# Kernel optimization log

Hardware: AMD Instinct MI355X
Metric: run time of the kernel (lower is better)

The kernel has to match this reference:

```python
import jax, jax.numpy as jnp
import numpy as np

EPS = 1e-6

def _ln(x):
    # LayerNorm without affine, eps=1e-6
    mu = jnp.mean(x, axis=-1, keepdims=True)
    var = jnp.var(x, axis=-1, keepdims=True)
    return (x - mu) * jax.lax.rsqrt(var + EPS)

def setup_inputs() -> dict:
    key = jax.random.key(0)
    ks = jax.random.split(key, 12)
    B, N, C = 8, 1024, 768
    H = 12
    Hf = 4 * C  # mlp hidden
    s = 0.02
    return {
        "x": jax.random.normal(ks[0], (B, N, C), jnp.float32),
        "c": jax.random.normal(ks[1], (B, C), jnp.float32),
        "qkv_w": jax.random.normal(ks[2], (3 * C, C), jnp.float32) * s,
        "qkv_b": jax.random.normal(ks[3], (3 * C,), jnp.float32) * s,
        "proj_w": jax.random.normal(ks[4], (C, C), jnp.float32) * s,
        "proj_b": jax.random.normal(ks[5], (C,), jnp.float32) * s,
        "fc1_w": jax.random.normal(ks[6], (Hf, C), jnp.float32) * s,
        "fc1_b": jax.random.normal(ks[7], (Hf,), jnp.float32) * s,
        "fc2_w": jax.random.normal(ks[8], (C, Hf), jnp.float32) * s,
        "fc2_b": jax.random.normal(ks[9], (C,), jnp.float32) * s,
        "ada_w": jax.random.normal(ks[10], (6 * C, C), jnp.float32) * s,
        "ada_b": jax.random.normal(ks[11], (6 * C,), jnp.float32) * s,
    }

def reference(x, c, qkv_w, qkv_b, proj_w, proj_b, fc1_w, fc1_b, fc2_w, fc2_b, ada_w, ada_b):
    B, N, C = x.shape
    H = 12
    D = C // H
    scale = D ** -0.5

    # adaLN_modulation: SiLU then Linear -> chunk into 6 [B, C] pieces
    ada = jax.nn.silu(c) @ ada_w.T + ada_b  # [B, 6C]
    sh_msa, sc_msa, g_msa, sh_mlp, sc_mlp, g_mlp = jnp.split(ada, 6, axis=1)

    def modulate(h, shift, scale_):
        return h * (1 + scale_[:, None, :]) + shift[:, None, :]

    # --- attention branch ---
    h = modulate(_ln(x), sh_msa, sc_msa)
    qkv = h @ qkv_w.T + qkv_b                       # [B, N, 3C]
    qkv = qkv.reshape(B, N, 3, H, D)
    q, k, v = qkv[:, :, 0], qkv[:, :, 1], qkv[:, :, 2]   # [B, N, H, D]
    attn = jnp.einsum('bnhd,bmhd->bhnm', q, k) * scale   # [B, H, N, N]
    attn = jax.nn.softmax(attn, axis=-1)
    o = jnp.einsum('bhnm,bmhd->bnhd', attn, v).reshape(B, N, C)
    o = o @ proj_w.T + proj_b
    x = x + g_msa[:, None, :] * o

    # --- MLP branch ---
    h = modulate(_ln(x), sh_mlp, sc_mlp)
    h = jax.nn.gelu(h @ fc1_w.T + fc1_b, approximate=False)
    h = h @ fc2_w.T + fc2_b
    x = x + g_mlp[:, None, :] * h
    return x
```

## Files before the change

kernel.cpp:

```cpp
#include <hip/hip_runtime.h>
#include <hip/hip_bf16.h>
#include <math.h>

typedef __attribute__((ext_vector_type(8))) short bf16x8;
typedef __attribute__((ext_vector_type(4))) float f32x4;

__device__ __forceinline__ unsigned short f2bf(float f) {
  union { float f; unsigned int u; } v; v.f = f;
  unsigned int u = v.u;
  u += 0x7fffu + ((u >> 16) & 1u);
  return (unsigned short)(u >> 16);
}

__device__ __forceinline__ void gl2l16(const unsigned short* g, unsigned short* l) {
  __builtin_amdgcn_global_load_lds(
      (const __attribute__((address_space(1))) unsigned int*)g,
      (__attribute__((address_space(3))) unsigned int*)l, 16, 0, 0);
}

__device__ __forceinline__ float gelu_fast(float v) {
  float arg = v * (1.59576912f + 0.07135481f * v * v);
  return v / (1.f + __expf(-arg));
}

__global__ __launch_bounds__(256) void k_conv(const float4* __restrict__ s0, ushort4* __restrict__ d0,
                                              const float4* __restrict__ s1, ushort4* __restrict__ d1,
                                              const float4* __restrict__ s2, ushort4* __restrict__ d2,
                                              const float4* __restrict__ s3, ushort4* __restrict__ d3) {
  int i = blockIdx.x * 256 + threadIdx.x;
  const float4* s; ushort4* d; int off;
  if (i < 442368) { s = s0; d = d0; off = i; }
  else if (i < 589824) { s = s1; d = d1; off = i - 442368; }
  else if (i < 1179648) { s = s2; d = d2; off = i - 589824; }
  else { s = s3; d = d3; off = i - 1179648; }
  float4 f = s[off];
  ushort4 o;
  o.x = f2bf(f.x); o.y = f2bf(f.y); o.z = f2bf(f.z); o.w = f2bf(f.w);
  d[off] = o;
}

__global__ __launch_bounds__(256) void k_ada(const float* __restrict__ c,
                                             const float* __restrict__ ada_w,
                                             const float* __restrict__ ada_b,
                                             float* __restrict__ ada) {
  __shared__ float sc[8 * 768];
  __shared__ float red[4][64][8];
  const int t = threadIdx.x;
  for (int i = t; i < 8 * 768; i += 256) {
    float v = c[i];
    sc[i] = v / (1.f + __expf(-v));
  }
  __syncthreads();
  const int cl = t & 63, ks = t >> 6;
  const int col = blockIdx.x * 64 + cl;
  float acc[8];
#pragma unroll
  for (int b = 0; b < 8; b++) acc[b] = 0.f;
  const float* wr = ada_w + (size_t)col * 768 + ks * 192;
  for (int k = 0; k < 192; k += 4) {
    float4 w = *(const float4*)&wr[k];
    const int kk = ks * 192 + k;
#pragma unroll
    for (int b = 0; b < 8; b++) {
      acc[b] += sc[b * 768 + kk] * w.x + sc[b * 768 + kk + 1] * w.y +
                sc[b * 768 + kk + 2] * w.z + sc[b * 768 + kk + 3] * w.w;
    }
  }
#pragma unroll
  for (int b = 0; b < 8; b++) red[ks][cl][b] = acc[b];
  __syncthreads();
  if (ks == 0) {
    const float bj = ada_b[col];
#pragma unroll
    for (int b = 0; b < 8; b++)
      ada[b * 4608 + col] = red[0][cl][b] + red[1][cl][b] + red[2][cl][b] + red[3][cl][b] + bj;
  }
}

__global__ __launch_bounds__(256) void k_ln_mod(const float* __restrict__ x,
                                                const float* __restrict__ ada,
                                                int sh_off, int sc_off,
                                                unsigned short* __restrict__ h) {
  const int row = blockIdx.x, t = threadIdx.x, b = row >> 10;
  const float* xr = x + (size_t)row * 768;
  float v0 = xr[t], v1 = xr[t + 256], v2 = xr[t + 512];
  float s = v0 + v1 + v2;
  float ss = v0 * v0 + v1 * v1 + v2 * v2;
#pragma unroll
  for (int m = 1; m < 64; m <<= 1) {
    s += __shfl_xor(s, m);
    ss += __shfl_xor(ss, m);
  }
  __shared__ float red[8];
  if ((t & 63) == 0) { red[t >> 6] = s; red[4 + (t >> 6)] = ss; }
  __syncthreads();
  const float S = red[0] + red[1] + red[2] + red[3];
  const float SS = red[4] + red[5] + red[6] + red[7];
  const float mean = S * (1.f / 768.f);
  const float var = SS * (1.f / 768.f) - mean * mean;
  const float inv = rsqrtf(var + 1e-6f);
  const float* sh = ada + b * 4608 + sh_off;
  const float* scp = ada + b * 4608 + sc_off;
  unsigned short* hr = h + (size_t)row * 768;
  float vv[3] = {v0, v1, v2};
#pragma unroll
  for (int i = 0; i < 3; i++) {
    int cx = t + i * 256;
    float hh = (vv[i] - mean) * inv;
    hh = hh * (1.f + scp[cx]) + sh[cx];
    hr[cx] = f2bf(hh);
  }
}

template <int EPI, int TN>
__global__ __launch_bounds__(256) void k_gemm(const unsigned short* __restrict__ A,
                                              const unsigned short* __restrict__ B,
                                              const float* __restrict__ bias,
                                              int N, int K, int nbx,
                                              const float* __restrict__ resid,
                                              const float* __restrict__ ada, int goff,
                                              float* __restrict__ outf,
                                              unsigned short* __restrict__ outb,
                                              unsigned short* __restrict__ vt) {
  constexpr int MI = (TN == 128) ? 4 : 2;
  __shared__ __align__(16) unsigned short Asm[2][128 * 32];
  __shared__ __align__(16) unsigned short Bsm[2][TN * 32];
  const int t = threadIdx.x;
  const int w = t >> 6, lane = t & 63, l = lane & 15, qd = lane >> 4;

  const int id = blockIdx.x;
  const int xcd = id & 7, jj = id >> 3;
  const int jm = jj / nbx;
  const int bmi = xcd + (jm << 3);
  const int bni = jj - jm * nbx;
  const int bn = bni * TN, bm = bmi * 128;

  const int wm = (TN == 128) ? (w >> 1) * 64 : w * 32;
  const int wn = (TN == 128) ? (w & 1) * 64 : 0;

  const int srow = t >> 2;
  const int scol = ((t & 3) ^ ((srow >> 1) & 3)) * 8;
  const unsigned short* Ap0 = A + (size_t)(bm + srow) * K + scol;
  const unsigned short* Ap1 = A + (size_t)(bm + 64 + srow) * K + scol;
  const unsigned short* Bp0 = B + (size_t)(bn + srow) * K + scol;
  const unsigned short* Bp1 = B + (size_t)(bn + 64 + srow) * K + scol;

  f32x4 acc[MI][4];
#pragma unroll
  for (int i = 0; i < MI; i++)
#pragma unroll
    for (int j = 0; j < 4; j++) acc[i][j] = {0.f, 0.f, 0.f, 0.f};

  const int swz = (l >> 1) & 3;

  for (int k0 = 0; k0 < K; k0 += 64) {
#pragma unroll
    for (int s = 0; s < 2; s++) {
      gl2l16(Ap0 + k0 + 32 * s, &Asm[s][w * 512]);
      gl2l16(Ap1 + k0 + 32 * s, &Asm[s][2048 + w * 512]);
      gl2l16(Bp0 + k0 + 32 * s, &Bsm[s][w * 512]);
      if (TN == 128) gl2l16(Bp1 + k0 + 32 * s, &Bsm[s][2048 + w * 512]);
    }
    __syncthreads();
#pragma unroll
    for (int s = 0; s < 2; s++) {
      bf16x8 af[MI], bfr[4];
#pragma unroll
      for (int i = 0; i < MI; i++)
        af[i] = *(const bf16x8*)&Asm[s][(wm + i * 16 + l) * 32 + ((qd ^ swz) << 3)];
#pragma unroll
      for (int j = 0; j < 4; j++)
        bfr[j] = *(const bf16x8*)&Bsm[s][(wn + j * 16 + l) * 32 + ((qd ^ swz) << 3)];
#pragma unroll
      for (int i = 0; i < MI; i++)
#pragma unroll
        for (int j = 0; j < 4; j++)
          acc[i][j] = __builtin_amdgcn_mfma_f32_16x16x32_bf16(af[i], bfr[j], acc[i][j], 0, 0, 0);
    }
    __syncthreads();
  }

#pragma unroll
  for (int i = 0; i < MI; i++) {
#pragma unroll
    for (int j = 0; j < 4; j++) {
      const int gn = bn + wn + j * 16 + l;
      const float bv = bias[gn];
#pragma unroll
      for (int r = 0; r < 4; r++) {
        const int gm = bm + wm + i * 16 + qd * 4 + r;
        float v = acc[i][j][r] + bv;
        if (EPI == 0) {
          if (gn < 1536) {
            outb[(size_t)gm * 1536 + gn] = f2bf(v);
          } else {
            const int hh = (gn - 1536) >> 6, dd = (gn - 1536) & 63;
            const int bb = gm >> 10, nn = gm & 1023;
            vt[(((size_t)bb * 12 + hh) * 64 + dd) * 1024 + nn] = f2bf(v);
          }
        } else if (EPI == 2) {
          outb[(size_t)gm * N + gn] = f2bf(gelu_fast(v));
        } else {
          const int bb = gm >> 10;
          const float g = ada[bb * 4608 + goff + gn];
          outf[(size_t)gm * 768 + gn] = resid[(size_t)gm * 768 + gn] + g * v;
        }
      }
    }
  }
}

__global__ __launch_bounds__(256) void k_attn(const unsigned short* __restrict__ qk,
                                              const unsigned short* __restrict__ vt,
                                              unsigned short* __restrict__ o) {
  __shared__ __align__(16) unsigned short Ksm[64 * 76];
  __shared__ __align__(16) unsigned short Vsm[64 * 76];
  __shared__ __align__(16) unsigned short Psm[128 * 76];
  const int t = threadIdx.x;
  const int id = blockIdx.x;
  const int xcd = id & 7, j = id >> 3;
  const int bh = xcd * 12 + (j >> 3);
  const int qb = j & 7;
  const int b = bh / 12, h = bh - b * 12;
  const int w = t >> 6, lane = t & 63, l = lane & 15, qd = lane >> 4;

  const size_t qrow0 = (size_t)(b * 1024 + qb * 128 + w * 32 + l);
  bf16x8 qf[2][2];
#pragma unroll
  for (int mt = 0; mt < 2; mt++)
#pragma unroll
    for (int ks = 0; ks < 2; ks++)
      qf[mt][ks] = *(const bf16x8*)&qk[(qrow0 + mt * 16) * 1536 + h * 64 + ks * 32 + qd * 8];

  f32x4 oacc[2][4];
  float rsum[2][4];
#pragma unroll
  for (int mt = 0; mt < 2; mt++)
#pragma unroll
    for (int j2 = 0; j2 < 4; j2++) { oacc[mt][j2] = {0.f, 0.f, 0.f, 0.f}; rsum[mt][j2] = 0.f; }

  const size_t kbase = (size_t)b * 1024 * 1536 + 768 + h * 64;
  const size_t vbase = ((size_t)(b * 12 + h)) * 64 * 1024;

  for (int k0 = 0; k0 < 1024; k0 += 64) {
    for (int idx = t; idx < 512; idx += 256) {
      const int row = idx >> 3, ch = (idx & 7) * 8;
      *(bf16x8*)&Ksm[row * 76 + ch] =
          *(const bf16x8*)&qk[kbase + (size_t)(k0 + row) * 1536 + ch];
      *(bf16x8*)&Vsm[row * 76 + ch] =
          *(const bf16x8*)&vt[vbase + (size_t)row * 1024 + k0 + ch];
    }
    __syncthreads();

    bf16x8 kf[4][2];
#pragma unroll
    for (int ct = 0; ct < 4; ct++)
#pragma unroll
      for (int ks = 0; ks < 2; ks++)
        kf[ct][ks] = *(const bf16x8*)&Ksm[(ct * 16 + l) * 76 + ks * 32 + qd * 8];

#pragma unroll
    for (int mt = 0; mt < 2; mt++) {
      f32x4 s[4];
#pragma unroll
      for (int ct = 0; ct < 4; ct++) {
        f32x4 a = {0.f, 0.f, 0.f, 0.f};
        a = __builtin_amdgcn_mfma_f32_16x16x32_bf16(qf[mt][0], kf[ct][0], a, 0, 0, 0);
        a = __builtin_amdgcn_mfma_f32_16x16x32_bf16(qf[mt][1], kf[ct][1], a, 0, 0, 0);
        s[ct] = a;
      }
#pragma unroll
      for (int ct = 0; ct < 4; ct++) {
#pragma unroll
        for (int r = 0; r < 4; r++) {
          float p = __expf(s[ct][r] * 0.125f);
          rsum[mt][r] += p;
          Psm[(w * 32 + mt * 16 + qd * 4 + r) * 76 + ct * 16 + l] = f2bf(p);
        }
      }
    }

    bf16x8 vf[4][2];
#pragma unroll
    for (int dt = 0; dt < 4; dt++)
#pragma unroll
      for (int ks = 0; ks < 2; ks++)
        vf[dt][ks] = *(const bf16x8*)&Vsm[(dt * 16 + l) * 76 + ks * 32 + qd * 8];
#pragma unroll
    for (int mt = 0; mt < 2; mt++) {
      bf16x8 pf0 = *(const bf16x8*)&Psm[(w * 32 + mt * 16 + l) * 76 + qd * 8];
      bf16x8 pf1 = *(const bf16x8*)&Psm[(w * 32 + mt * 16 + l) * 76 + 32 + qd * 8];
#pragma unroll
      for (int dt = 0; dt < 4; dt++) {
        oacc[mt][dt] = __builtin_amdgcn_mfma_f32_16x16x32_bf16(pf0, vf[dt][0], oacc[mt][dt], 0, 0, 0);
        oacc[mt][dt] = __builtin_amdgcn_mfma_f32_16x16x32_bf16(pf1, vf[dt][1], oacc[mt][dt], 0, 0, 0);
      }
    }
    __syncthreads();
  }

#pragma unroll
  for (int mt = 0; mt < 2; mt++)
#pragma unroll
    for (int r = 0; r < 4; r++) {
      float rs = rsum[mt][r];
#pragma unroll
      for (int mk = 1; mk < 16; mk <<= 1) rs += __shfl_xor(rs, mk);
      const float inv = 1.f / rs;
      const size_t orow = (size_t)(b * 1024 + qb * 128 + w * 32 + mt * 16 + qd * 4 + r);
#pragma unroll
      for (int dt = 0; dt < 4; dt++)
        o[orow * 768 + h * 64 + dt * 16 + l] = f2bf(oacc[mt][dt][r] * inv);
    }
}

extern "C" void kernel_launch(void* const* d_in, const int* in_sizes, int n_in,
                              void* d_out, int out_size, void* d_ws, size_t ws_size,
                              hipStream_t stream) {
  const float* x      = (const float*)d_in[0];
  const float* c      = (const float*)d_in[1];
  const float* qkv_w  = (const float*)d_in[2];
  const float* qkv_b  = (const float*)d_in[3];
  const float* proj_w = (const float*)d_in[4];
  const float* proj_b = (const float*)d_in[5];
  const float* fc1_w  = (const float*)d_in[6];
  const float* fc1_b  = (const float*)d_in[7];
  const float* fc2_w  = (const float*)d_in[8];
  const float* fc2_b  = (const float*)d_in[9];
  const float* ada_w  = (const float*)d_in[10];
  const float* ada_b  = (const float*)d_in[11];
  float* out = (float*)d_out;

  char* ws = (char*)d_ws;
  float*          ada       = (float*)(ws + 0);
  unsigned short* qkv_w_bf  = (unsigned short*)(ws + 147456);
  unsigned short* proj_w_bf = (unsigned short*)(ws + 3686400);
  unsigned short* fc1_w_bf  = (unsigned short*)(ws + 4866048);
  unsigned short* fc2_w_bf  = (unsigned short*)(ws + 9584640);
  unsigned short* h_bf      = (unsigned short*)(ws + 14303232);
  unsigned short* qk_bf     = (unsigned short*)(ws + 26886144);
  unsigned short* vt_bf     = (unsigned short*)(ws + 52051968);
  unsigned short* o_bf      = (unsigned short*)(ws + 64634880);
  float*          x1        = (float*)(ws + 77217792);
  unsigned short* f1_bf     = qk_bf;

  k_conv<<<6912, 256, 0, stream>>>((const float4*)qkv_w, (ushort4*)qkv_w_bf,
                                   (const float4*)proj_w, (ushort4*)proj_w_bf,
                                   (const float4*)fc1_w, (ushort4*)fc1_w_bf,
                                   (const float4*)fc2_w, (ushort4*)fc2_w_bf);

  k_ada<<<72, 256, 0, stream>>>(c, ada_w, ada_b, ada);

  k_ln_mod<<<8192, 256, 0, stream>>>(x, ada, 0, 768, h_bf);

  k_gemm<0, 128><<<18 * 64, 256, 0, stream>>>(h_bf, qkv_w_bf, qkv_b, 2304, 768, 18,
                                              nullptr, nullptr, 0, nullptr, qk_bf, vt_bf);

  k_attn<<<768, 256, 0, stream>>>(qk_bf, vt_bf, o_bf);

  k_gemm<1, 64><<<12 * 64, 256, 0, stream>>>(o_bf, proj_w_bf, proj_b, 768, 768, 12,
                                             x, ada, 1536, x1, nullptr, nullptr);

  k_ln_mod<<<8192, 256, 0, stream>>>(x1, ada, 2304, 3072, h_bf);

  k_gemm<2, 128><<<24 * 64, 256, 0, stream>>>(h_bf, fc1_w_bf, fc1_b, 3072, 768, 24,
                                              nullptr, nullptr, 0, nullptr, f1_bf, nullptr);

  k_gemm<3, 64><<<12 * 64, 256, 0, stream>>>(f1_bf, fc2_w_bf, fc2_b, 768, 3072, 12,
                                             x1, ada, 3840, out, nullptr, nullptr);
}
```

Measured before the change: 421.3 us.

## Store intermediate residual in bf16, merge prologue kernels, use 3D attention grid

The intermediate residual x1 is now written and read as bf16 rather than fp32, which halves its memory traffic in the proj epilogue, the second LayerNorm and the fc2 epilogue. The weight conversion kernel and the adaLN modulation kernel are merged into one prologue launch to save a kernel launch. The attention kernel switches from XCD-aware block swizzling to a plain 3D grid. Keeping the residual in bf16 lowers the precision of the output's residual path, and dropping the swizzle may reduce L2 locality on K/V.

```diff
diff --git a/kernel.cpp b/kernel.cpp
--- a/kernel.cpp
+++ b/kernel.cpp
@@ -12,6 +12,11 @@
   return (unsigned short)(u >> 16);
 }
 
+__device__ __forceinline__ float bf2f(unsigned short h) {
+  union { unsigned int u; float f; } v; v.u = ((unsigned int)h) << 16;
+  return v.f;
+}
+
 __device__ __forceinline__ void gl2l16(const unsigned short* g, unsigned short* l) {
   __builtin_amdgcn_global_load_lds(
       (const __attribute__((address_space(1))) unsigned int*)g,
@@ -23,36 +28,38 @@
   return v / (1.f + __expf(-arg));
 }
 
-__global__ __launch_bounds__(256) void k_conv(const float4* __restrict__ s0, ushort4* __restrict__ d0,
-                                              const float4* __restrict__ s1, ushort4* __restrict__ d1,
-                                              const float4* __restrict__ s2, ushort4* __restrict__ d2,
-                                              const float4* __restrict__ s3, ushort4* __restrict__ d3) {
-  int i = blockIdx.x * 256 + threadIdx.x;
-  const float4* s; ushort4* d; int off;
-  if (i < 442368) { s = s0; d = d0; off = i; }
-  else if (i < 589824) { s = s1; d = d1; off = i - 442368; }
-  else if (i < 1179648) { s = s2; d = d2; off = i - 589824; }
-  else { s = s3; d = d3; off = i - 1179648; }
-  float4 f = s[off];
-  ushort4 o;
-  o.x = f2bf(f.x); o.y = f2bf(f.y); o.z = f2bf(f.z); o.w = f2bf(f.w);
-  d[off] = o;
-}
-
-__global__ __launch_bounds__(256) void k_ada(const float* __restrict__ c,
-                                             const float* __restrict__ ada_w,
-                                             const float* __restrict__ ada_b,
-                                             float* __restrict__ ada) {
-  __shared__ float sc[8 * 768];
-  __shared__ float red[4][64][8];
+__global__ __launch_bounds__(256) void k_prologue(
+    const float4* __restrict__ s0, ushort4* __restrict__ d0,
+    const float4* __restrict__ s1, ushort4* __restrict__ d1,
+    const float4* __restrict__ s2, ushort4* __restrict__ d2,
+    const float4* __restrict__ s3, ushort4* __restrict__ d3,
+    const float* __restrict__ c, const float* __restrict__ ada_w,
+    const float* __restrict__ ada_b, float* __restrict__ ada) {
+  __shared__ float smem[8 * 768 + 4 * 64 * 8];
   const int t = threadIdx.x;
+  const int id = blockIdx.x;
+  if (id < 6912) {
+    int i = id * 256 + t;
+    const float4* s; ushort4* d; int off;
+    if (i < 442368) { s = s0; d = d0; off = i; }
+    else if (i < 589824) { s = s1; d = d1; off = i - 442368; }
+    else if (i < 1179648) { s = s2; d = d2; off = i - 589824; }
+    else { s = s3; d = d3; off = i - 1179648; }
+    float4 f = s[off];
+    ushort4 o;
+    o.x = f2bf(f.x); o.y = f2bf(f.y); o.z = f2bf(f.z); o.w = f2bf(f.w);
+    d[off] = o;
+    return;
+  }
+  float* sc = smem;
+  float* red = smem + 8 * 768;
   for (int i = t; i < 8 * 768; i += 256) {
     float v = c[i];
     sc[i] = v / (1.f + __expf(-v));
   }
   __syncthreads();
   const int cl = t & 63, ks = t >> 6;
-  const int col = blockIdx.x * 64 + cl;
+  const int col = (id - 6912) * 64 + cl;
   float acc[8];
 #pragma unroll
   for (int b = 0; b < 8; b++) acc[b] = 0.f;
@@ -67,23 +74,31 @@
     }
   }
 #pragma unroll
-  for (int b = 0; b < 8; b++) red[ks][cl][b] = acc[b];
+  for (int b = 0; b < 8; b++) red[(ks * 64 + cl) * 8 + b] = acc[b];
   __syncthreads();
   if (ks == 0) {
     const float bj = ada_b[col];
 #pragma unroll
     for (int b = 0; b < 8; b++)
-      ada[b * 4608 + col] = red[0][cl][b] + red[1][cl][b] + red[2][cl][b] + red[3][cl][b] + bj;
-  }
-}
-
-__global__ __launch_bounds__(256) void k_ln_mod(const float* __restrict__ x,
+      ada[b * 4608 + col] = red[(0 * 64 + cl) * 8 + b] + red[(1 * 64 + cl) * 8 + b] +
+                            red[(2 * 64 + cl) * 8 + b] + red[(3 * 64 + cl) * 8 + b] + bj;
+  }
+}
+
+template <bool BF>
+__global__ __launch_bounds__(256) void k_ln_mod(const void* __restrict__ xin,
                                                 const float* __restrict__ ada,
                                                 int sh_off, int sc_off,
                                                 unsigned short* __restrict__ h) {
   const int row = blockIdx.x, t = threadIdx.x, b = row >> 10;
-  const float* xr = x + (size_t)row * 768;
-  float v0 = xr[t], v1 = xr[t + 256], v2 = xr[t + 512];
+  float v0, v1, v2;
+  if (BF) {
+    const unsigned short* xr = (const unsigned short*)xin + (size_t)row * 768;
+    v0 = bf2f(xr[t]); v1 = bf2f(xr[t + 256]); v2 = bf2f(xr[t + 512]);
+  } else {
+    const float* xr = (const float*)xin + (size_t)row * 768;
+    v0 = xr[t]; v1 = xr[t + 256]; v2 = xr[t + 512];
+  }
   float s = v0 + v1 + v2;
   float ss = v0 * v0 + v1 * v1 + v2 * v2;
 #pragma unroll
@@ -117,7 +132,8 @@
                                               const unsigned short* __restrict__ B,
                                               const float* __restrict__ bias,
                                               int N, int K, int nbx,
-                                              const float* __restrict__ resid,
+                                              const float* __restrict__ residf,
+                                              const unsigned short* __restrict__ residb,
                                               const float* __restrict__ ada, int goff,
                                               float* __restrict__ outf,
                                               unsigned short* __restrict__ outb,
@@ -198,12 +214,18 @@
             const int bb = gm >> 10, nn = gm & 1023;
             vt[(((size_t)bb * 12 + hh) * 64 + dd) * 1024 + nn] = f2bf(v);
           }
+        } else if (EPI == 1) {
+          const int bb = gm >> 10;
+          const float g = ada[bb * 4608 + goff + gn];
+          outb[(size_t)gm * 768 + gn] =
+              f2bf(residf[(size_t)gm * 768 + gn] + g * v);
         } else if (EPI == 2) {
           outb[(size_t)gm * N + gn] = f2bf(gelu_fast(v));
         } else {
           const int bb = gm >> 10;
           const float g = ada[bb * 4608 + goff + gn];
-          outf[(size_t)gm * 768 + gn] = resid[(size_t)gm * 768 + gn] + g * v;
+          outf[(size_t)gm * 768 + gn] =
+              bf2f(residb[(size_t)gm * 768 + gn]) + g * v;
         }
       }
     }
@@ -217,11 +239,7 @@
   __shared__ __align__(16) unsigned short Vsm[64 * 76];
   __shared__ __align__(16) unsigned short Psm[128 * 76];
   const int t = threadIdx.x;
-  const int id = blockIdx.x;
-  const int xcd = id & 7, j = id >> 3;
-  const int bh = xcd * 12 + (j >> 3);
-  const int qb = j & 7;
-  const int b = bh / 12, h = bh - b * 12;
+  const int qb = blockIdx.x, h = blockIdx.y, b = blockIdx.z;
   const int w = t >> 6, lane = t & 63, l = lane & 15, qd = lane >> 4;
 
   const size_t qrow0 = (size_t)(b * 1024 + qb * 128 + w * 32 + l);
@@ -341,31 +359,34 @@
   unsigned short* qk_bf     = (unsigned short*)(ws + 26886144);
   unsigned short* vt_bf     = (unsigned short*)(ws + 52051968);
   unsigned short* o_bf      = (unsigned short*)(ws + 64634880);
-  float*          x1        = (float*)(ws + 77217792);
+  unsigned short* x1_bf     = (unsigned short*)(ws + 77217792);
   unsigned short* f1_bf     = qk_bf;
 
-  k_conv<<<6912, 256, 0, stream>>>((const float4*)qkv_w, (ushort4*)qkv_w_bf,
-                                   (const float4*)proj_w, (ushort4*)proj_w_bf,
-                                   (const float4*)fc1_w, (ushort4*)fc1_w_bf,
-                                   (const float4*)fc2_w, (ushort4*)fc2_w_bf);
-
-  k_ada<<<72, 256, 0, stream>>>(c, ada_w, ada_b, ada);
-
-  k_ln_mod<<<8192, 256, 0, stream>>>(x, ada, 0, 768, h_bf);
+  k_prologue<<<6984, 256, 0, stream>>>((const float4*)qkv_w, (ushort4*)qkv_w_bf,
+                                       (const float4*)proj_w, (ushort4*)proj_w_bf,
+                                       (const float4*)fc1_w, (ushort4*)fc1_w_bf,
+                                       (const float4*)fc2_w, (ushort4*)fc2_w_bf,
+                                       c, ada_w, ada_b, ada);
+
+  k_ln_mod<false><<<8192, 256, 0, stream>>>(x, ada, 0, 768, h_bf);
 
   k_gemm<0, 128><<<18 * 64, 256, 0, stream>>>(h_bf, qkv_w_bf, qkv_b, 2304, 768, 18,
-                                              nullptr, nullptr, 0, nullptr, qk_bf, vt_bf);
-
-  k_attn<<<768, 256, 0, stream>>>(qk_bf, vt_bf, o_bf);
+                                              nullptr, nullptr, nullptr, 0,
+                                              nullptr, qk_bf, vt_bf);
+
+  k_attn<<<dim3(8, 12, 8), 256, 0, stream>>>(qk_bf, vt_bf, o_bf);
 
   k_gemm<1, 64><<<12 * 64, 256, 0, stream>>>(o_bf, proj_w_bf, proj_b, 768, 768, 12,
-                                             x, ada, 1536, x1, nullptr, nullptr);
-
-  k_ln_mod<<<8192, 256, 0, stream>>>(x1, ada, 2304, 3072, h_bf);
+                                             x, nullptr, ada, 1536,
+                                             nullptr, x1_bf, nullptr);
+
+  k_ln_mod<true><<<8192, 256, 0, stream>>>(x1_bf, ada, 2304, 3072, h_bf);
 
   k_gemm<2, 128><<<24 * 64, 256, 0, stream>>>(h_bf, fc1_w_bf, fc1_b, 3072, 768, 24,
-                                              nullptr, nullptr, 0, nullptr, f1_bf, nullptr);
+                                              nullptr, nullptr, nullptr, 0,
+                                              nullptr, f1_bf, nullptr);
 
   k_gemm<3, 64><<<12 * 64, 256, 0, stream>>>(f1_bf, fc2_w_bf, fc2_b, 768, 3072, 12,
-                                             x1, ada, 3840, out, nullptr, nullptr);
-}
+                                             nullptr, x1_bf, ada, 3840,
+                                             out, nullptr, nullptr);
+}
```

Result: no change. 419.5 us (-0.4%).
